# Kernel tuning notes

Hardware: AMD Instinct MI355X
Metric: run time of the kernel (lower is better)

## Reference

```python
import jax, jax.numpy as jnp
import numpy as np

B, N_HEADS, DIM, Z, X = 128, 12, 768, 7, 14


def _rpe_index(z, x):
    """2D concatenated self-attention relative positional encoding index.
    Tokens = z*z template tokens followed by x*x search tokens. Two token
    pairs share a bias index iff they have the same (dh, dw, region_i, region_j).
    """
    zh, zw = np.meshgrid(np.arange(z), np.arange(z), indexing='ij')
    xh, xw = np.meshgrid(np.arange(x), np.arange(x), indexing='ij')
    h = np.concatenate([zh.ravel(), xh.ravel()])
    w = np.concatenate([zw.ravel(), xw.ravel()])
    region = np.concatenate([np.zeros(z * z, np.int64), np.ones(x * x, np.int64)])
    dh = h[:, None] - h[None, :]
    dw = w[:, None] - w[None, :]
    rb = np.broadcast_to(region[:, None], dh.shape)
    rc = np.broadcast_to(region[None, :], dh.shape)
    key = np.stack([dh, dw, rb, rc], axis=-1).reshape(-1, 4)
    _, inv = np.unique(key, axis=0, return_inverse=True)
    return inv.reshape(dh.shape)  # (N, N) int


def setup_inputs() -> dict:
    key = jax.random.key(0)
    ks = jax.random.split(key, 4)
    N = Z * Z + X * X  # 245
    idx = _rpe_index(Z, X)
    n_bias = int(idx.max()) + 1
    return {
        "x": jax.random.normal(ks[0], (B, N, DIM), jnp.float32),
        "qkv_w": jax.random.normal(ks[1], (3 * DIM, DIM), jnp.float32) * 0.02,
        "proj_w": jax.random.normal(ks[2], (DIM, DIM), jnp.float32) * 0.02,
        "proj_b": jnp.zeros((DIM,), jnp.float32),
        "bias_table": jax.random.normal(ks[3], (N_HEADS, n_bias), jnp.float32) * 0.02,
        "rel_index": jnp.asarray(idx, jnp.int32),
    }


def reference(x, qkv_w, proj_w, proj_b, bias_table, rel_index):
    Bq, N, C = x.shape
    H = N_HEADS
    Dh = C // H
    scale = Dh ** -0.5
    # qkv projection (no bias): (B, N, 3, H, Dh)
    qkv = (x @ qkv_w.T).reshape(Bq, N, 3, H, Dh)
    q = jnp.moveaxis(qkv[:, :, 0], 2, 1)  # (B, H, N, Dh)
    k = jnp.moveaxis(qkv[:, :, 1], 2, 1)
    v = jnp.moveaxis(qkv[:, :, 2], 2, 1)
    attn = jnp.einsum('bhnd,bhmd->bhnm', q, k) * scale  # (B, H, N, N)
    # relative position bias gather: (H, N, N) broadcast over batch
    attn = attn + bias_table[:, rel_index][None]
    attn = jax.nn.softmax(attn, axis=-1)
    out = jnp.einsum('bhnm,bhmd->bhnd', attn, v)  # (B, H, N, Dh)
    out = jnp.moveaxis(out, 1, 2).reshape(Bq, N, C)
    return out @ proj_w.T + proj_b
```

## Files before the change

### kernel.cpp

```cpp
#include <hip/hip_runtime.h>
#include <hip/hip_bf16.h>
#include <stdint.h>

#define BATCH 128
#define NTOK 245
#define HEADS 12
#define DHEAD 64
#define CDIM 768
#define KT 24
#define SUBT 512

typedef __attribute__((ext_vector_type(8))) short short8;
typedef __attribute__((ext_vector_type(4))) float f32x4;

__device__ __forceinline__ float bf2f(uint32_t hbits) {
    union { uint32_t u; float f; } v; v.u = hbits << 16; return v.f;
}
__device__ __forceinline__ uint32_t f2bf(float f) {
    union { float f; uint32_t u; } v; v.f = f;
    return (v.u + 0x7fffu + ((v.u >> 16) & 1u)) >> 16;
}
__device__ __forceinline__ ushort2 pk2bf(float x, float y) {
    union { __hip_bfloat162 h; ushort2 u; } c;
    c.h = __float22bfloat162_rn(make_float2(x, y));
    return c.u;
}
__device__ __forceinline__ size_t tiled_addr(int m, int k) {
    return (((size_t)(m >> 4) * KT + (k >> 5)) * 64 + ((k >> 3) & 3) * 16 + (m & 15)) * 8
           + (k & 7);
}
__device__ __forceinline__ void gl_lds16(const uint16_t* g, ushort* lds) {
    __builtin_amdgcn_global_load_lds(
        (const __attribute__((address_space(1))) void*)g,
        (__attribute__((address_space(3))) void*)lds,
        16, 0, 0);
}

__global__ __launch_bounds__(256)
void cvt_tile_bf16(const float* __restrict__ src, uint16_t* __restrict__ dst, int n8)
{
    int i = blockIdx.x * 256 + threadIdx.x;
    const int stride = gridDim.x * 256;
    for (; i < n8; i += stride) {
        const int sl = i & 63;
        const int tile = i >> 6;
        const int rt = tile / KT, kt = tile - rt * KT;
        const size_t soff = (size_t)(rt * 16 + (sl & 15)) * CDIM + kt * 32 + (sl >> 4) * 8;
        float4 a = *(const float4*)(src + soff);
        float4 b = *(const float4*)(src + soff + 4);
        ushort2 p0 = pk2bf(a.x, a.y), p1 = pk2bf(a.z, a.w);
        ushort2 p2 = pk2bf(b.x, b.y), p3 = pk2bf(b.z, b.w);
        uint4 o;
        o.x = (uint32_t)p0.x | ((uint32_t)p0.y << 16);
        o.y = (uint32_t)p1.x | ((uint32_t)p1.y << 16);
        o.z = (uint32_t)p2.x | ((uint32_t)p2.y << 16);
        o.w = (uint32_t)p3.x | ((uint32_t)p3.y << 16);
        *(uint4*)(dst + (size_t)i * 8) = o;
    }
}

__global__ __launch_bounds__(256)
void bias_pre(const float* __restrict__ bias_table, const int* __restrict__ rel,
              int n_bias, uint16_t* __restrict__ bias_t)
{
    const int h = blockIdx.x, j = blockIdx.y, q = threadIdx.x;
    float v = -30000.f;
    if (j < NTOK && q < NTOK) v = bias_table[(size_t)h * n_bias + rel[q * NTOK + j]];
    bias_t[((size_t)h * 256 + j) * 256 + q] = (uint16_t)f2bf(v);
}

#define GEMM_STEP(CUR, kt)                                                      \
    {                                                                           \
        __syncthreads();                                                        \
        if ((kt) < KT - 1) {                                                    \
            const int ko = ((kt) + 1) * SUBT;                                   \
            gl_lds16(gA0 + ko, &Af[(CUR)^1][w  ][0][0]);                        \
            gl_lds16(gA1 + ko, &Af[(CUR)^1][w+4][0][0]);                        \
            gl_lds16(gB0 + ko, &Bf[(CUR)^1][w  ][0][0]);                        \
            gl_lds16(gB1 + ko, &Bf[(CUR)^1][w+4][0][0]);                        \
        }                                                                       \
        short8 af[4], bf[4];                                                    \
        _Pragma("unroll")                                                       \
        for (int m = 0; m < 4; ++m)                                             \
            af[m] = *(const short8*)&Af[CUR][wr*4 + m][l][0];                   \
        _Pragma("unroll")                                                       \
        for (int n = 0; n < 4; ++n)                                             \
            bf[n] = *(const short8*)&Bf[CUR][wc*4 + n][l][0];                   \
        _Pragma("unroll")                                                       \
        for (int m = 0; m < 4; ++m)                                             \
            _Pragma("unroll")                                                   \
            for (int n = 0; n < 4; ++n)                                         \
                acc[m][n] = __builtin_amdgcn_mfma_f32_16x16x32_bf16(bf[n], af[m], acc[m][n], 0, 0, 0); \
    }

__global__ __launch_bounds__(256)
void qkv_gemm_mfma(const uint16_t* __restrict__ xb, const uint16_t* __restrict__ wq,
                   uint16_t* __restrict__ qkv)
{
    __shared__ ushort Af[2][8][64][8];
    __shared__ ushort Bf[2][8][64][8];
    const int t = threadIdx.x;
    const int w = t >> 6, l = t & 63;
    const int wr = w >> 1, wc = w & 1;
    const int lm = l & 15, lk = l >> 4;

    const int bid = blockIdx.x;
    const int xcd = bid & 7;
    const int wg = (xcd < 2 ? xcd * 552 : 1104 + (xcd - 2) * 551) + (bid >> 3);
    const int mtile = wg / 18, ctile = wg - mtile * 18;
    const int m0 = mtile * 128, c0 = ctile * 128;

    const uint16_t* gA0 = xb + ((size_t)(mtile*8 + w    ) * KT * 64 + l) * 8;
    const uint16_t* gA1 = xb + ((size_t)(mtile*8 + w + 4) * KT * 64 + l) * 8;
    const uint16_t* gB0 = wq + ((size_t)(ctile*8 + w    ) * KT * 64 + l) * 8;
    const uint16_t* gB1 = wq + ((size_t)(ctile*8 + w + 4) * KT * 64 + l) * 8;

    f32x4 acc[4][4];
    #pragma unroll
    for (int m = 0; m < 4; ++m)
        #pragma unroll
        for (int n = 0; n < 4; ++n) acc[m][n] = (f32x4){0.f,0.f,0.f,0.f};

    gl_lds16(gA0, &Af[0][w  ][0][0]);
    gl_lds16(gA1, &Af[0][w+4][0][0]);
    gl_lds16(gB0, &Bf[0][w  ][0][0]);
    gl_lds16(gB1, &Bf[0][w+4][0][0]);

    #pragma unroll 1
    for (int kt = 0; kt < KT; kt += 2) {
        GEMM_STEP(0, kt);
        GEMM_STEP(1, kt + 1);
    }

    int sArr[4], hArr[4], dArr[4];
    #pragma unroll
    for (int n = 0; n < 4; ++n) {
        int c = c0 + wc*64 + n*16 + lk*4;
        int s = c / CDIM; int rem = c - s * CDIM;
        sArr[n] = s; hArr[n] = rem >> 6; dArr[n] = rem & 63;
    }
    #pragma unroll
    for (int m = 0; m < 4; ++m) {
        int gm  = m0 + wr*64 + m*16 + lm;
        int b   = gm / NTOK;
        int tok = gm - b * NTOK;
        #pragma unroll
        for (int n = 0; n < 4; ++n) {
            ushort2 u0 = pk2bf(acc[m][n][0], acc[m][n][1]);
            ushort2 u1 = pk2bf(acc[m][n][2], acc[m][n][3]);
            uint2 pk;
            pk.x = (uint32_t)u0.x | ((uint32_t)u0.y << 16);
            pk.y = (uint32_t)u1.x | ((uint32_t)u1.y << 16);
            size_t addr = ((((size_t)b*3 + sArr[n])*HEADS + hArr[n])*NTOK + tok)*DHEAD + dArr[n];
            *(uint2*)(qkv + addr) = pk;
        }
    }
}

__global__ __launch_bounds__(512)
void attn_mfma(const uint16_t* __restrict__ qkv, const uint16_t* __restrict__ bias_t,
               uint16_t* __restrict__ o_t)
{
    __shared__ ushort Ks[256][72];
    __shared__ ushort Vt[64][264];
    __shared__ ushort Ps[8][16][72];
    const int bh = blockIdx.x;
    const int b = bh / HEADS, h = bh % HEADS;
    const int t = threadIdx.x;
    const int w = t >> 6, l = t & 63;
    const int lm = l & 15, lk = l >> 4;
    const int wq0 = w * 32;

    const uint16_t* qbase = qkv + (((size_t)b*3 + 0)*HEADS + h) * (NTOK*DHEAD);
    const uint16_t* kbase = qkv + (((size_t)b*3 + 1)*HEADS + h) * (NTOK*DHEAD);
    const uint16_t* vbase = qkv + (((size_t)b*3 + 2)*HEADS + h) * (NTOK*DHEAD);
    const uint16_t* btab  = bias_t + (size_t)h * 256 * 256;

    {
        const int col = (t & 7) * 8;
        #pragma unroll
        for (int p = 0; p < 4; ++p) {
            int row = p * 64 + (t >> 3);
            uint4 val = make_uint4(0u,0u,0u,0u);
            if (row < NTOK) val = *(const uint4*)(kbase + (size_t)row * DHEAD + col);
            *(uint4*)&Ks[row][col] = val;
        }
    }
    {
        const int j  = t >> 1;
        const int dh = (t & 1) * 32;
        uint4 r0 = make_uint4(0,0,0,0), r1 = r0, r2 = r0, r3 = r0;
        if (j < NTOK) {
            const uint16_t* src = vbase + (size_t)j * DHEAD + dh;
            r0 = *(const uint4*)(src);
            r1 = *(const uint4*)(src + 8);
            r2 = *(const uint4*)(src + 16);
            r3 = *(const uint4*)(src + 24);
        }
        union { uint4 v[4]; ushort s[32]; } u;
        u.v[0] = r0; u.v[1] = r1; u.v[2] = r2; u.v[3] = r3;
        #pragma unroll
        for (int i = 0; i < 32; ++i)
            Vt[dh + i][j] = u.s[i];
    }

    short8 qf[2][2];
    #pragma unroll
    for (int m = 0; m < 2; ++m) {
        int qrow = wq0 + m*16 + lm; if (qrow > NTOK-1) qrow = NTOK-1;
        #pragma unroll
        for (int k2 = 0; k2 < 2; ++k2)
            qf[m][k2] = *(const short8*)(qbase + (size_t)qrow * DHEAD + k2*32 + lk*8);
    }

    f32x4 acc_o[2][4];
    float lsum[2][4];
    #pragma unroll
    for (int m = 0; m < 2; ++m) {
        #pragma unroll
        for (int n = 0; n < 4; ++n) acc_o[m][n] = (f32x4){0.f,0.f,0.f,0.f};
        #pragma unroll
        for (int r = 0; r < 4; ++r) lsum[m][r] = 0.f;
    }

    __syncthreads();

    for (int jb = 0; jb < 4; ++jb) {
        short8 kf[4][2], vf[4][2];
        #pragma unroll
        for (int n = 0; n < 4; ++n)
            #pragma unroll
            for (int k2 = 0; k2 < 2; ++k2) {
                kf[n][k2] = *(const short8*)&Ks[jb*64 + n*16 + lm][k2*32 + lk*8];
                vf[n][k2] = *(const short8*)&Vt[n*16 + lm][jb*64 + k2*32 + lk*8];
            }

        #pragma unroll
        for (int m = 0; m < 2; ++m) {
            f32x4 sv[4];
            #pragma unroll
            for (int n = 0; n < 4; ++n) {
                f32x4 z = (f32x4){0.f,0.f,0.f,0.f};
                sv[n] = __builtin_amdgcn_mfma_f32_16x16x32_bf16(qf[m][0], kf[n][0], z, 0, 0, 0);
                sv[n] = __builtin_amdgcn_mfma_f32_16x16x32_bf16(qf[m][1], kf[n][1], sv[n], 0, 0, 0);
            }
            #pragma unroll
            for (int n = 0; n < 4; ++n) {
                uint2 bb = *(const uint2*)(btab + (size_t)(jb*64 + n*16 + lm) * 256 + wq0 + m*16 + lk*4);
                float s0 = fmaf(sv[n][0], 0.125f, bf2f(bb.x & 0xffffu));
                float s1 = fmaf(sv[n][1], 0.125f, bf2f(bb.x >> 16));
                float s2 = fmaf(sv[n][2], 0.125f, bf2f(bb.y & 0xffffu));
                float s3 = fmaf(sv[n][3], 0.125f, bf2f(bb.y >> 16));
                sv[n][0] = __expf(fminf(s0, 30.f));
                sv[n][1] = __expf(fminf(s1, 30.f));
                sv[n][2] = __expf(fminf(s2, 30.f));
                sv[n][3] = __expf(fminf(s3, 30.f));
            }
            #pragma unroll
            for (int n = 0; n < 4; ++n)
                #pragma unroll
                for (int r = 0; r < 4; ++r) {
                    ushort u = (ushort)f2bf(sv[n][r]);
                    lsum[m][r] += bf2f(u);
                    Ps[w][lk*4 + r][n*16 + lm] = u;
                }
            short8 pf[2];
            #pragma unroll
            for (int k2 = 0; k2 < 2; ++k2)
                pf[k2] = *(const short8*)&Ps[w][lm][k2*32 + lk*8];
            #pragma unroll
            for (int n = 0; n < 4; ++n) {
                acc_o[m][n] = __builtin_amdgcn_mfma_f32_16x16x32_bf16(pf[0], vf[n][0], acc_o[m][n], 0, 0, 0);
                acc_o[m][n] = __builtin_amdgcn_mfma_f32_16x16x32_bf16(pf[1], vf[n][1], acc_o[m][n], 0, 0, 0);
            }
        }
    }

    #pragma unroll
    for (int m = 0; m < 2; ++m) {
        float inv[4];
        #pragma unroll
        for (int r = 0; r < 4; ++r) {
            float s = lsum[m][r];
            s += __shfl_xor(s, 1);
            s += __shfl_xor(s, 2);
            s += __shfl_xor(s, 4);
            s += __shfl_xor(s, 8);
            inv[r] = 1.f / s;
        }
        #pragma unroll
        for (int r = 0; r < 4; ++r) {
            int q = wq0 + m*16 + lk*4 + r;
            if (q < NTOK) {
                int gm = b * NTOK + q;
                #pragma unroll
                for (int n = 0; n < 4; ++n) {
                    int k = h * DHEAD + n*16 + lm;
                    o_t[tiled_addr(gm, k)] = (uint16_t)f2bf(acc_o[m][n][r] * inv[r]);
                }
            }
        }
    }
}

__global__ __launch_bounds__(256)
void proj_gemm_mfma(const uint16_t* __restrict__ ot, const uint16_t* __restrict__ wp,
                    const float* __restrict__ bias, float* __restrict__ out)
{
    __shared__ ushort Af[2][8][64][8];
    __shared__ ushort Bf[2][8][64][8];
    const int t = threadIdx.x;
    const int w = t >> 6, l = t & 63;
    const int wr = w >> 1, wc = w & 1;
    const int lm = l & 15, lk = l >> 4;

    const int bid = blockIdx.x;
    const int xcd = bid & 7;
    const int wg = (xcd < 6 ? xcd * 184 : 1104 + (xcd - 6) * 183) + (bid >> 3);
    const int mtile = wg / 6, ctile = wg - mtile * 6;
    const int m0 = mtile * 128, c0 = ctile * 128;

    const uint16_t* gA0 = ot + ((size_t)(mtile*8 + w    ) * KT * 64 + l) * 8;
    const uint16_t* gA1 = ot + ((size_t)(mtile*8 + w + 4) * KT * 64 + l) * 8;
    const uint16_t* gB0 = wp + ((size_t)(ctile*8 + w    ) * KT * 64 + l) * 8;
    const uint16_t* gB1 = wp + ((size_t)(ctile*8 + w + 4) * KT * 64 + l) * 8;

    f32x4 acc[4][4];
    #pragma unroll
    for (int m = 0; m < 4; ++m)
        #pragma unroll
        for (int n = 0; n < 4; ++n) acc[m][n] = (f32x4){0.f,0.f,0.f,0.f};

    gl_lds16(gA0, &Af[0][w  ][0][0]);
    gl_lds16(gA1, &Af[0][w+4][0][0]);
    gl_lds16(gB0, &Bf[0][w  ][0][0]);
    gl_lds16(gB1, &Bf[0][w+4][0][0]);

    #pragma unroll 1
    for (int kt = 0; kt < KT; kt += 2) {
        GEMM_STEP(0, kt);
        GEMM_STEP(1, kt + 1);
    }

    float4 bsv[4]; int cArr[4];
    #pragma unroll
    for (int n = 0; n < 4; ++n) {
        cArr[n] = c0 + wc*64 + n*16 + lk*4;
        bsv[n]  = *(const float4*)(bias + cArr[n]);
    }
    #pragma unroll
    for (int m = 0; m < 4; ++m) {
        int gm = m0 + wr*64 + m*16 + lm;
        #pragma unroll
        for (int n = 0; n < 4; ++n) {
            float4 r;
            r.x = acc[m][n][0] + bsv[n].x;
            r.y = acc[m][n][1] + bsv[n].y;
            r.z = acc[m][n][2] + bsv[n].z;
            r.w = acc[m][n][3] + bsv[n].w;
            *(float4*)(out + (size_t)gm * CDIM + cArr[n]) = r;
        }
    }
}

extern "C" void kernel_launch(void* const* d_in, const int* in_sizes, int n_in,
                              void* d_out, int out_size, void* d_ws, size_t ws_size,
                              hipStream_t stream)
{
    (void)n_in; (void)out_size;
    const float* x          = (const float*)d_in[0];
    const float* qkv_w      = (const float*)d_in[1];
    const float* proj_w     = (const float*)d_in[2];
    const float* proj_b     = (const float*)d_in[3];
    const float* bias_table = (const float*)d_in[4];
    const int*   rel        = (const int*)d_in[5];
    const int n_bias = in_sizes[4] / HEADS;

    const size_t qkv_elems = (size_t)BATCH * 3 * HEADS * NTOK * DHEAD;
    const size_t o_elems   = (size_t)BATCH * HEADS * NTOK * DHEAD;
    const size_t bt_elems  = (size_t)HEADS * 256 * 256;
    const size_t wq_elems  = (size_t)3 * CDIM * CDIM;
    const size_t wp_elems  = (size_t)CDIM * CDIM;

    uint16_t* qkv_ws = (uint16_t*)d_ws;
    uint16_t* o_ws   = qkv_ws + qkv_elems;
    uint16_t* bt_ws  = o_ws + o_elems;
    uint16_t* wq_ws  = bt_ws + bt_elems;
    uint16_t* wp_ws  = wq_ws + wq_elems;
    const size_t need = (qkv_elems + o_elems + bt_elems + wq_elems + wp_elems) * sizeof(uint16_t);
    if (ws_size < need) return;

    uint16_t* xb = o_ws;

    cvt_tile_bf16<<<2048, 256, 0, stream>>>(x, xb, (int)(o_elems / 8));
    cvt_tile_bf16<<<864, 256, 0, stream>>>(qkv_w, wq_ws, (int)(wq_elems / 8));
    cvt_tile_bf16<<<288, 256, 0, stream>>>(proj_w, wp_ws, (int)(wp_elems / 8));

    bias_pre<<<dim3(HEADS, 256), 256, 0, stream>>>(bias_table, rel, n_bias, bt_ws);

    qkv_gemm_mfma<<<4410, 256, 0, stream>>>(xb, wq_ws, qkv_ws);

    attn_mfma<<<dim3(BATCH * HEADS), 512, 0, stream>>>(qkv_ws, bt_ws, o_ws);

    proj_gemm_mfma<<<1470, 256, 0, stream>>>(o_ws, wp_ws, proj_b, (float*)d_out);
}
```

Before: 377.8 us.

## Triple-buffer GEMM LDS tiles with prefetch distance two and explicit vmcnt waits

Both MFMA GEMM kernels (QKV and output projection) move from a double-buffered LDS pipeline to a three-stage ring that keeps two K-tiles of global-to-LDS loads in flight. Each iteration waits with a partial vmcnt(4) plus a raw s_barrier instead of a full __syncthreads drain. The aim is to hide global load latency behind the MFMA work. In exchange, LDS use per block rises from 32KB to 48KB, which may lower occupancy, and the hand-written waitcnt depends on exactly four loads being issued per stage.

```diff
diff --git a/kernel.cpp b/kernel.cpp
--- a/kernel.cpp
+++ b/kernel.cpp
@@ -69,36 +69,50 @@
     bias_t[((size_t)h * 256 + j) * 256 + q] = (uint16_t)f2bf(v);
 }
 
-#define GEMM_STEP(CUR, kt)                                                      \
-    {                                                                           \
-        __syncthreads();                                                        \
-        if ((kt) < KT - 1) {                                                    \
-            const int ko = ((kt) + 1) * SUBT;                                   \
-            gl_lds16(gA0 + ko, &Af[(CUR)^1][w  ][0][0]);                        \
-            gl_lds16(gA1 + ko, &Af[(CUR)^1][w+4][0][0]);                        \
-            gl_lds16(gB0 + ko, &Bf[(CUR)^1][w  ][0][0]);                        \
-            gl_lds16(gB1 + ko, &Bf[(CUR)^1][w+4][0][0]);                        \
-        }                                                                       \
-        short8 af[4], bf[4];                                                    \
-        _Pragma("unroll")                                                       \
-        for (int m = 0; m < 4; ++m)                                             \
-            af[m] = *(const short8*)&Af[CUR][wr*4 + m][l][0];                   \
-        _Pragma("unroll")                                                       \
-        for (int n = 0; n < 4; ++n)                                             \
-            bf[n] = *(const short8*)&Bf[CUR][wc*4 + n][l][0];                   \
-        _Pragma("unroll")                                                       \
-        for (int m = 0; m < 4; ++m)                                             \
-            _Pragma("unroll")                                                   \
-            for (int n = 0; n < 4; ++n)                                         \
+#define GEMM_LOOP                                                                \
+    gl_lds16(gA0, &Af[0][w  ][0][0]);                                            \
+    gl_lds16(gA1, &Af[0][w+4][0][0]);                                            \
+    gl_lds16(gB0, &Bf[0][w  ][0][0]);                                            \
+    gl_lds16(gB1, &Bf[0][w+4][0][0]);                                            \
+    gl_lds16(gA0 + SUBT, &Af[1][w  ][0][0]);                                     \
+    gl_lds16(gA1 + SUBT, &Af[1][w+4][0][0]);                                     \
+    gl_lds16(gB0 + SUBT, &Bf[1][w  ][0][0]);                                     \
+    gl_lds16(gB1 + SUBT, &Bf[1][w+4][0][0]);                                     \
+    int cur = 0, nxt = 2;                                                        \
+    _Pragma("unroll 1")                                                          \
+    for (int t = 0; t < KT; ++t) {                                               \
+        if (t == KT - 1) { asm volatile("s_waitcnt vmcnt(0) lgkmcnt(0)" ::: "memory"); } \
+        else             { asm volatile("s_waitcnt vmcnt(4) lgkmcnt(0)" ::: "memory"); } \
+        __builtin_amdgcn_s_barrier();                                            \
+        if (t + 2 < KT) {                                                        \
+            const int ko = (t + 2) * SUBT;                                       \
+            gl_lds16(gA0 + ko, &Af[nxt][w  ][0][0]);                             \
+            gl_lds16(gA1 + ko, &Af[nxt][w+4][0][0]);                             \
+            gl_lds16(gB0 + ko, &Bf[nxt][w  ][0][0]);                             \
+            gl_lds16(gB1 + ko, &Bf[nxt][w+4][0][0]);                             \
+        }                                                                        \
+        short8 af[4], bf[4];                                                     \
+        _Pragma("unroll")                                                        \
+        for (int m = 0; m < 4; ++m)                                              \
+            af[m] = *(const short8*)&Af[cur][wr*4 + m][l][0];                    \
+        _Pragma("unroll")                                                        \
+        for (int n = 0; n < 4; ++n)                                              \
+            bf[n] = *(const short8*)&Bf[cur][wc*4 + n][l][0];                    \
+        _Pragma("unroll")                                                        \
+        for (int m = 0; m < 4; ++m)                                              \
+            _Pragma("unroll")                                                    \
+            for (int n = 0; n < 4; ++n)                                          \
                 acc[m][n] = __builtin_amdgcn_mfma_f32_16x16x32_bf16(bf[n], af[m], acc[m][n], 0, 0, 0); \
+        cur = (cur == 2) ? 0 : cur + 1;                                          \
+        nxt = (nxt == 2) ? 0 : nxt + 1;                                          \
     }
 
 __global__ __launch_bounds__(256)
 void qkv_gemm_mfma(const uint16_t* __restrict__ xb, const uint16_t* __restrict__ wq,
                    uint16_t* __restrict__ qkv)
 {
-    __shared__ ushort Af[2][8][64][8];
-    __shared__ ushort Bf[2][8][64][8];
+    __shared__ ushort Af[3][8][64][8];
+    __shared__ ushort Bf[3][8][64][8];
     const int t = threadIdx.x;
     const int w = t >> 6, l = t & 63;
     const int wr = w >> 1, wc = w & 1;
@@ -121,16 +135,7 @@
         #pragma unroll
         for (int n = 0; n < 4; ++n) acc[m][n] = (f32x4){0.f,0.f,0.f,0.f};
 
-    gl_lds16(gA0, &Af[0][w  ][0][0]);
-    gl_lds16(gA1, &Af[0][w+4][0][0]);
-    gl_lds16(gB0, &Bf[0][w  ][0][0]);
-    gl_lds16(gB1, &Bf[0][w+4][0][0]);
-
-    #pragma unroll 1
-    for (int kt = 0; kt < KT; kt += 2) {
-        GEMM_STEP(0, kt);
-        GEMM_STEP(1, kt + 1);
-    }
+    GEMM_LOOP
 
     int sArr[4], hArr[4], dArr[4];
     #pragma unroll
@@ -307,8 +312,8 @@
 void proj_gemm_mfma(const uint16_t* __restrict__ ot, const uint16_t* __restrict__ wp,
                     const float* __restrict__ bias, float* __restrict__ out)
 {
-    __shared__ ushort Af[2][8][64][8];
-    __shared__ ushort Bf[2][8][64][8];
+    __shared__ ushort Af[3][8][64][8];
+    __shared__ ushort Bf[3][8][64][8];
     const int t = threadIdx.x;
     const int w = t >> 6, l = t & 63;
     const int wr = w >> 1, wc = w & 1;
@@ -331,16 +336,7 @@
         #pragma unroll
         for (int n = 0; n < 4; ++n) acc[m][n] = (f32x4){0.f,0.f,0.f,0.f};
 
-    gl_lds16(gA0, &Af[0][w  ][0][0]);
-    gl_lds16(gA1, &Af[0][w+4][0][0]);
-    gl_lds16(gB0, &Bf[0][w  ][0][0]);
-    gl_lds16(gB1, &Bf[0][w+4][0][0]);
-
-    #pragma unroll 1
-    for (int kt = 0; kt < KT; kt += 2) {
-        GEMM_STEP(0, kt);
-        GEMM_STEP(1, kt + 1);
-    }
+    GEMM_LOOP
 
     float4 bsv[4]; int cArr[4];
     #pragma unroll
```

After: 322.1 us. 1.17x faster.
